# Kernel tuning notes

Measured on AMD Instinct MI355X. Metric: run time of the kernel, lower is better.

## Reference

```python
import jax, jax.numpy as jnp
import numpy as np

EPS = 1e-7  # K.epsilon()

_LC = np.zeros((3, 3, 3), np.float32)  # Levi-Civita for 1x1->1
_LC[0, 1, 2] = _LC[1, 2, 0] = _LC[2, 0, 1] = 1.0
_LC[0, 2, 1] = _LC[2, 1, 0] = _LC[1, 0, 2] = -1.0


def _ssp(x):
    # shifted softplus: log(0.5*exp(x)+0.5)
    return jnp.log(0.5 * jnp.exp(x) + 0.5)


def _radial(image, w1, b1, w2, b2):
    # Sequential([Dense(32), Dense(feat)]) -- linear Dense layers (no activation)
    return (image @ w1 + b1) @ w2 + b2  # (m, a, b, feat)


def setup_inputs() -> dict:
    key = jax.random.key(0)
    ks = jax.random.split(key, 16)
    M, A, RBF, F, SI, H = 4, 256, 64, 32, 32, 32
    inp = {}
    inp["image"] = jax.random.uniform(ks[0], (M, A, A, RBF), dtype=jnp.float32)
    inp["vectors"] = jax.random.normal(ks[1], (M, A, A, 3), dtype=jnp.float32)
    inp["feat0"] = jax.random.normal(ks[2], (M, A, F, 1), dtype=jnp.float32)
    inp["feat1"] = jax.random.normal(ks[3], (M, A, F, 3), dtype=jnp.float32)
    i = 4
    for rin in (0, 1):
        for fro in (0, 1):
            tag = f"{rin}{fro}"
            inp[f"w1_{tag}"] = jax.random.normal(ks[i], (RBF, H)) / np.sqrt(RBF).astype(np.float32)
            inp[f"b1_{tag}"] = jnp.zeros((H,), jnp.float32)
            i += 1
            inp[f"w2_{tag}"] = jax.random.normal(ks[i], (H, F)) / np.sqrt(np.float32(H))
            inp[f"b2_{tag}"] = jnp.zeros((F,), jnp.float32)
            i += 1
    inp["w_si0"] = jax.random.normal(ks[i], (SI, 2 * F)) / np.sqrt(np.float32(2 * F)); i += 1
    inp["w_si1"] = jax.random.normal(ks[i], (SI, 3 * F)) / np.sqrt(np.float32(3 * F)); i += 1
    inp["b_act0"] = jnp.zeros((SI,), jnp.float32)
    inp["b_act1"] = jnp.zeros((SI,), jnp.float32)
    return inp


def reference(image, vectors, feat0, feat1,
              w1_00, b1_00, w2_00, b2_00,
              w1_01, b1_01, w2_01, b2_01,
              w1_10, b1_10, w2_10, b2_10,
              w1_11, b1_11, w2_11, b2_11,
              w_si0, w_si1, b_act0, b_act1):
    # mask where |r_ab| < eps (self-pairs / padding)
    mask = (jnp.sqrt(jnp.sum(vectors * vectors, axis=-1)) < EPS)[..., None]  # (m,a,b,1)

    def filt0(w1, b1, w2, b2):
        return _radial(image, w1, b1, w2, b2)  # (m,a,b,F), implicit rep index of size 1

    def filt1(w1, b1, w2, b2):
        r = jnp.where(mask, 0.0, _radial(image, w1, b1, w2, b2))  # masked radial
        return vectors[:, :, :, None, :] * r[..., None]  # (m,a,b,F,3)

    f0_in0 = filt0(w1_00, b1_00, w2_00, b2_00)
    f1_in0 = filt1(w1_01, b1_01, w2_01, b2_01)
    f0_in1 = filt0(w1_10, b1_10, w2_10, b2_10)
    f1_in1 = filt1(w1_11, b1_11, w2_11, b2_11)

    # point convolution (sum over neighbor atoms b)
    out_0x0_0 = jnp.einsum('mabf,mbfj->mafj', f0_in0, feat0)   # (m,a,F,1)
    out_0x1_1 = jnp.einsum('mabfi,mbfj->mafi', f1_in0, feat0)  # (m,a,F,3)
    out_1x0_1 = jnp.einsum('mabf,mbfj->mafj', f0_in1, feat1)   # (m,a,F,3)
    cg0 = jnp.eye(3, dtype=image.dtype)[None]                  # (1,3,3): 1x1->0
    out_1x1_0 = jnp.einsum('ijk,mabfj,mbfk->mafi', cg0, f1_in1, feat1)  # (m,a,F,1)
    lc = jnp.asarray(_LC, image.dtype)                         # 1x1->1
    out_1x1_1 = jnp.einsum('ijk,mabfj,mbfk->mafi', lc, f1_in1, feat1)   # (m,a,F,3)

    # concat along channel dim per output RO
    cat0 = jnp.concatenate([out_0x0_0, out_1x1_0], axis=2)  # (m,a,2F,1)
    cat1 = jnp.concatenate([out_0x1_1, out_1x0_1, out_1x1_1], axis=2)  # (m,a,3F,3)

    # self-interaction: einsum('mafi,gf->maig') then transpose -> (m,a,g,i)
    si0 = jnp.einsum('mafi,gf->magi', cat0, w_si0)  # (m,a,SI,1)
    si1 = jnp.einsum('mafi,gf->magi', cat1, w_si1)  # (m,a,SI,3)

    # equivariant activation
    o0 = _ssp(si0 + b_act0[None, None, :, None])
    n1 = jnp.sqrt(jnp.maximum(jnp.sum(si1 * si1, axis=-1), EPS))  # norm_with_epsilon
    a1 = _ssp(n1 + b_act1)
    o1 = si1 * (a1 / n1)[..., None]
    return (o0, o1)
```

## Files before the change

kernel.cpp:

```cpp
#include <hip/hip_runtime.h>
#include <math.h>

#define M_ 4
#define A_ 256
#define RBF_ 64
#define F_ 32
#define H_ 32
#define SI_ 32
#define TF_ 128

typedef __attribute__((ext_vector_type(8))) short bf16x8;
typedef __attribute__((ext_vector_type(4))) float f32x4;
typedef __attribute__((ext_vector_type(3))) float f32x3;

__device__ __forceinline__ unsigned short f2bf(float f) {
  union { float f; unsigned u; } v; v.f = f;
  unsigned r = v.u + 0x7FFFu + ((v.u >> 16) & 1u);
  return (unsigned short)(r >> 16);
}

__device__ __forceinline__ unsigned pack2bf(float lo, float hi) {
  union { float f; unsigned u; } a, b; a.f = lo; b.f = hi;
  return __builtin_amdgcn_perm(b.u + 0x8000u, a.u + 0x8000u, 0x07060302u);
}

__device__ __forceinline__ float sspf(float x) {
  return fmaxf(x, 0.f) + log1pf(expf(-fabsf(x))) - 0.6931471805599453f;
}

__global__ __launch_bounds__(256) void combine_weights(
    const float* __restrict__ w1_00, const float* __restrict__ b1_00,
    const float* __restrict__ w2_00, const float* __restrict__ b2_00,
    const float* __restrict__ w1_01, const float* __restrict__ b1_01,
    const float* __restrict__ w2_01, const float* __restrict__ b2_01,
    const float* __restrict__ w1_10, const float* __restrict__ b1_10,
    const float* __restrict__ w2_10, const float* __restrict__ b2_10,
    const float* __restrict__ w1_11, const float* __restrict__ b1_11,
    const float* __restrict__ w2_11, const float* __restrict__ b2_11,
    unsigned short* __restrict__ wsT, float* __restrict__ bcw)
{
  const float* w1s[4] = {w1_00, w1_01, w1_10, w1_11};
  const float* b1s[4] = {b1_00, b1_01, b1_10, b1_11};
  const float* w2s[4] = {w2_00, w2_01, w2_10, w2_11};
  const float* b2s[4] = {b2_00, b2_01, b2_10, b2_11};
  int tid = blockIdx.x * 256 + threadIdx.x;
  int k   = tid >> 7;
  int tf  = tid & 127;
  int tag = tf >> 5, f = tf & 31;
  const float* w1 = w1s[tag];
  const float* w2 = w2s[tag];
  float s = 0.f;
  for (int h = 0; h < H_; ++h) s += w1[k * H_ + h] * w2[h * F_ + f];
  wsT[tf * 64 + k] = f2bf(s);
  if (tid < TF_) {
    const float* b1 = b1s[tag];
    const float* b2 = b2s[tag];
    float sb = b2[f];
    for (int h = 0; h < H_; ++h) sb += b1[h] * w2[h * F_ + f];
    bcw[tf] = sb;
  }
}

__global__ __launch_bounds__(512, 4) void conv_partial(
    const float* __restrict__ image, const float* __restrict__ vectors,
    const float* __restrict__ feat0, const float* __restrict__ feat1,
    const unsigned short* __restrict__ wsT, const float* __restrict__ bcw,
    float* __restrict__ part)
{
  __shared__ __align__(16) unsigned short sA[128 * 72];
  __shared__ float sV[128 * 3];

  const int t    = threadIdx.x;
  const int bid  = blockIdx.x;
  const int ma   = bid >> 1;
  const int half = bid & 1;
  const int m    = ma >> 8;
  const int l    = t & 63;
  const int n    = l & 15;
  const int quad = l >> 4;
  const int wu    = __builtin_amdgcn_readfirstlane(t >> 6);
  const int role  = (wu + ((bid & 3) << 1)) & 7;
  const int which = role & 1;
  const int tag   = role >> 1;
  const int ct    = tag * 2 + which;
  const int f     = which * 16 + n;

  const unsigned short* wr = wsT + (ct * 16 + n) * 64 + quad * 8;
  const bf16x8 w0 = *(const bf16x8*)(wr);
  const bf16x8 w1 = *(const bf16x8*)(wr + 32);
  const float  bc = bcw[ct * 16 + n];

  const float* imgH = image + ((size_t)ma * A_ + half * 128) * RBF_;
  #pragma unroll
  for (int i = 0; i < 2; ++i) {
    int g = t + 512 * i;
    int r = g >> 3, c8 = g & 7;
    const float* src = imgH + r * RBF_ + c8 * 8;
    float4 v0 = *(const float4*)(src);
    float4 v1 = *(const float4*)(src + 4);
    uint4 pk;
    pk.x = pack2bf(v0.x, v0.y);
    pk.y = pack2bf(v0.z, v0.w);
    pk.z = pack2bf(v1.x, v1.y);
    pk.w = pack2bf(v1.z, v1.w);
    *(uint4*)&sA[r * 72 + c8 * 8] = pk;
  }
  if (t < 384) sV[t] = vectors[((size_t)ma * A_ + half * 128) * 3 + t];

  const int b0q = half * 128 + quad * 4;
  const float* p0c = feat0 + (size_t)(m * A_ + b0q) * F_ + f;
  const float* p1c = feat1 + ((size_t)(m * A_ + b0q) * F_ + f) * 3;
  const float* svc = &sV[quad * 4 * 3];
  const unsigned short* aBc = &sA[n * 72 + quad * 8];

  float gx[2][4], gy[2][4], gz[2][4];
  float pA = 0.f, pB0 = 0.f, pB1 = 0.f, pB2 = 0.f;

#define PF(BUF) { \
    if (tag <= 1) { \
      _Pragma("unroll") \
      for (int r = 0; r < 4; ++r) gx[BUF][r] = p0c[r * F_]; \
    } else { \
      _Pragma("unroll") \
      for (int r = 0; r < 4; ++r) { \
        f32x3 v = *(const f32x3*)(p1c + r * (F_ * 3)); \
        gx[BUF][r] = v[0]; gy[BUF][r] = v[1]; gz[BUF][r] = v[2]; \
      } \
    } \
    p0c += 16 * F_; p1c += 16 * F_ * 3; }

#define BODY(AOFF, SOFF, GX, GY, GZ) { \
    const bf16x8 a0 = *(const bf16x8*)(aBc + (AOFF)); \
    const bf16x8 a1 = *(const bf16x8*)(aBc + (AOFF) + 32); \
    f32x4 acc = {bc, bc, bc, bc}; \
    acc = __builtin_amdgcn_mfma_f32_16x16x32_bf16(a0, w0, acc, 0, 0, 0); \
    acc = __builtin_amdgcn_mfma_f32_16x16x32_bf16(a1, w1, acc, 0, 0, 0); \
    if (tag == 0) {             \
      _Pragma("unroll") \
      for (int r = 0; r < 4; ++r) pA += acc[r] * GX[r]; \
    } else if (tag == 1) {      \
      _Pragma("unroll") \
      for (int r = 0; r < 4; ++r) { \
        const float s = acc[r] * GX[r]; \
        pB0 += svc[(SOFF) + r * 3 + 0] * s; \
        pB1 += svc[(SOFF) + r * 3 + 1] * s; \
        pB2 += svc[(SOFF) + r * 3 + 2] * s; \
      } \
    } else if (tag == 2) {      \
      _Pragma("unroll") \
      for (int r = 0; r < 4; ++r) { \
        const float Rr = acc[r]; \
        pB0 += Rr * GX[r]; pB1 += Rr * GY[r]; pB2 += Rr * GZ[r]; \
      } \
    } else {                    \
      _Pragma("unroll") \
      for (int r = 0; r < 4; ++r) { \
        const float Rr = acc[r]; \
        const float ax = GX[r], ay = GY[r], az = GZ[r]; \
        const float vx = svc[(SOFF) + r * 3 + 0]; \
        const float vy = svc[(SOFF) + r * 3 + 1]; \
        const float vz = svc[(SOFF) + r * 3 + 2]; \
        float d = vx * ax; d = fmaf(vy, ay, d); d = fmaf(vz, az, d); \
        pA = fmaf(Rr, d, pA); \
        float c0 = vy * az; c0 = fmaf(-vz, ay, c0); pB0 = fmaf(Rr, c0, pB0); \
        float c1 = vz * ax; c1 = fmaf(-vx, az, c1); pB1 = fmaf(Rr, c1, pB1); \
        float c2 = vx * ay; c2 = fmaf(-vy, ax, c2); pB2 = fmaf(Rr, c2, pB2); \
      } \
    } }

  PF(0)
  __syncthreads();

  #pragma unroll 1
  for (int it = 0; it < 4; ++it) {
    PF(1)
    BODY(0, 0, gx[0], gy[0], gz[0])
    if (it < 3) PF(0)
    BODY(1152, 48, gx[1], gy[1], gz[1])
    aBc += 2 * 1152;
    svc += 2 * 48;
  }

#define QRED(x) { x += __shfl_xor(x, 16); x += __shfl_xor(x, 32); }
  QRED(pA) QRED(pB0) QRED(pB1) QRED(pB2)
  if (quad == 0) {
    float* dst = part + ((size_t)ma * 2 + half) * 352;
    if (tag == 0) {
      dst[f] = pA;
    } else if (tag == 1) {
      f32x3 v = {pB0, pB1, pB2};
      *(f32x3*)&dst[64 + f * 3] = v;
    } else if (tag == 2) {
      f32x3 v = {pB0, pB1, pB2};
      *(f32x3*)&dst[160 + f * 3] = v;
    } else {
      dst[32 + f] = pA;
      f32x3 v = {pB0, pB1, pB2};
      *(f32x3*)&dst[256 + f * 3] = v;
    }
  }
}

__global__ __launch_bounds__(64) void si_epilogue(
    const float* __restrict__ part,
    const float* __restrict__ w_si0, const float* __restrict__ w_si1,
    const float* __restrict__ b_act0, const float* __restrict__ b_act1,
    float* __restrict__ out)
{
  __shared__ float cat[352];
  const int ma = blockIdx.x;
  const int t  = threadIdx.x;
  const float* pA = part + (size_t)ma * 704;
  const float* pB = pA + 352;
  for (int s = t; s < 352; s += 64) cat[s] = pA[s] + pB[s];
  __syncthreads();

  const int outBase = ma * SI_;
  if (t < 32) {
    const float* wr = w_si0 + t * 64;
    float s = 0.f;
    #pragma unroll 8
    for (int ff = 0; ff < 64; ++ff) s += cat[ff] * wr[ff];
    s += b_act0[t];
    out[outBase + t] = sspf(s);
  } else {
    int g = t - 32;
    const float* wr = w_si1 + g * 96;
    float s0 = 0.f, s1 = 0.f, s2 = 0.f;
    #pragma unroll 8
    for (int ff = 0; ff < 96; ++ff) {
      float wv = wr[ff];
      s0 += cat[64 + ff * 3 + 0] * wv;
      s1 += cat[64 + ff * 3 + 1] * wv;
      s2 += cat[64 + ff * 3 + 2] * wv;
    }
    float n2 = s0 * s0 + s1 * s1 + s2 * s2;
    float n1 = sqrtf(fmaxf(n2, 1e-7f));
    float a1 = sspf(n1 + b_act1[g]);
    float sc = a1 / n1;
    int ob = M_ * A_ * SI_ + (outBase + g) * 3;
    out[ob + 0] = s0 * sc;
    out[ob + 1] = s1 * sc;
    out[ob + 2] = s2 * sc;
  }
}

extern "C" void kernel_launch(void* const* d_in, const int* in_sizes, int n_in,
                              void* d_out, int out_size, void* d_ws, size_t ws_size,
                              hipStream_t stream) {
  const float* image   = (const float*)d_in[0];
  const float* vectors = (const float*)d_in[1];
  const float* feat0   = (const float*)d_in[2];
  const float* feat1   = (const float*)d_in[3];
  const float* w_si0   = (const float*)d_in[20];
  const float* w_si1   = (const float*)d_in[21];
  const float* b_act0  = (const float*)d_in[22];
  const float* b_act1  = (const float*)d_in[23];
  unsigned short* wsT = (unsigned short*)d_ws;
  float* bcw  = (float*)((char*)d_ws + 16384);
  float* part = (float*)((char*)d_ws + 32768);
  float* out  = (float*)d_out;

  combine_weights<<<32, 256, 0, stream>>>(
      (const float*)d_in[4],  (const float*)d_in[5],
      (const float*)d_in[6],  (const float*)d_in[7],
      (const float*)d_in[8],  (const float*)d_in[9],
      (const float*)d_in[10], (const float*)d_in[11],
      (const float*)d_in[12], (const float*)d_in[13],
      (const float*)d_in[14], (const float*)d_in[15],
      (const float*)d_in[16], (const float*)d_in[17],
      (const float*)d_in[18], (const float*)d_in[19],
      wsT, bcw);

  conv_partial<<<2 * M_ * A_, 512, 0, stream>>>(
      image, vectors, feat0, feat1, wsT, bcw, part);

  si_epilogue<<<M_ * A_, 64, 0, stream>>>(
      part, w_si0, w_si1, b_act0, b_act1, out);
}
```

Baseline: 161.3 us.

## Deepen feature prefetch to three buffers and stagger tile order per wave

The feature prefetch grows from two buffers to three, and the 8-step loop over b-tiles is fully unrolled. Each wave now starts at a different tile, offset by its wave index, which spreads LDS and global access across waves. Vector reads from shared memory become aligned float4 loads, and accumulations are written as explicit FMAs. The launch bound drops the minimum blocks per SM from 4 to 3, allowing more registers for the deeper buffering at the cost of possible lower occupancy.

```diff
diff --git a/kernel.cpp b/kernel.cpp
--- a/kernel.cpp
+++ b/kernel.cpp
@@ -61,14 +61,14 @@
   }
 }
 
-__global__ __launch_bounds__(512, 4) void conv_partial(
+__global__ __launch_bounds__(512, 3) void conv_partial(
     const float* __restrict__ image, const float* __restrict__ vectors,
     const float* __restrict__ feat0, const float* __restrict__ feat1,
     const unsigned short* __restrict__ wsT, const float* __restrict__ bcw,
     float* __restrict__ part)
 {
   __shared__ __align__(16) unsigned short sA[128 * 72];
-  __shared__ float sV[128 * 3];
+  __shared__ __align__(16) float sV[128 * 3];
 
   const int t    = threadIdx.x;
   const int bid  = blockIdx.x;
@@ -107,59 +107,73 @@
   }
   if (t < 384) sV[t] = vectors[((size_t)ma * A_ + half * 128) * 3 + t];
 
-  const int b0q = half * 128 + quad * 4;
-  const float* p0c = feat0 + (size_t)(m * A_ + b0q) * F_ + f;
-  const float* p1c = feat1 + ((size_t)(m * A_ + b0q) * F_ + f) * 3;
-  const float* svc = &sV[quad * 4 * 3];
-  const unsigned short* aBc = &sA[n * 72 + quad * 8];
-
-  float gx[2][4], gy[2][4], gz[2][4];
+  const int bq = half * 128 + quad * 4;
+  const float* p0b = feat0 + (size_t)(m * A_ + bq) * F_ + f;
+  const float* p1b = feat1 + ((size_t)(m * A_ + bq) * F_ + f) * 3;
+
+  float gx[3][4], gy[3][4], gz[3][4];
   float pA = 0.f, pB0 = 0.f, pB1 = 0.f, pB2 = 0.f;
 
-#define PF(BUF) { \
+#define PF(BUF, TJ) { \
+    const int _tj = (TJ); \
     if (tag <= 1) { \
-      _Pragma("unroll") \
-      for (int r = 0; r < 4; ++r) gx[BUF][r] = p0c[r * F_]; \
+      const float* pp = p0b + _tj * (16 * F_); \
+      _Pragma("unroll") \
+      for (int r = 0; r < 4; ++r) gx[BUF][r] = pp[r * F_]; \
     } else { \
-      _Pragma("unroll") \
-      for (int r = 0; r < 4; ++r) { \
-        f32x3 v = *(const f32x3*)(p1c + r * (F_ * 3)); \
+      const float* pp = p1b + _tj * (16 * F_ * 3); \
+      _Pragma("unroll") \
+      for (int r = 0; r < 4; ++r) { \
+        f32x3 v = *(const f32x3*)(pp + r * (F_ * 3)); \
         gx[BUF][r] = v[0]; gy[BUF][r] = v[1]; gz[BUF][r] = v[2]; \
       } \
-    } \
-    p0c += 16 * F_; p1c += 16 * F_ * 3; }
-
-#define BODY(AOFF, SOFF, GX, GY, GZ) { \
-    const bf16x8 a0 = *(const bf16x8*)(aBc + (AOFF)); \
-    const bf16x8 a1 = *(const bf16x8*)(aBc + (AOFF) + 32); \
+    } }
+
+#define BODY(BUF, TJ) { \
+    const int _tj = (TJ); \
+    const unsigned short* ap = &sA[(_tj * 16 + n) * 72 + quad * 8]; \
+    const bf16x8 a0 = *(const bf16x8*)(ap); \
+    const bf16x8 a1 = *(const bf16x8*)(ap + 32); \
     f32x4 acc = {bc, bc, bc, bc}; \
     acc = __builtin_amdgcn_mfma_f32_16x16x32_bf16(a0, w0, acc, 0, 0, 0); \
     acc = __builtin_amdgcn_mfma_f32_16x16x32_bf16(a1, w1, acc, 0, 0, 0); \
     if (tag == 0) {             \
       _Pragma("unroll") \
-      for (int r = 0; r < 4; ++r) pA += acc[r] * GX[r]; \
+      for (int r = 0; r < 4; ++r) pA += acc[r] * gx[BUF][r]; \
     } else if (tag == 1) {      \
-      _Pragma("unroll") \
-      for (int r = 0; r < 4; ++r) { \
-        const float s = acc[r] * GX[r]; \
-        pB0 += svc[(SOFF) + r * 3 + 0] * s; \
-        pB1 += svc[(SOFF) + r * 3 + 1] * s; \
-        pB2 += svc[(SOFF) + r * 3 + 2] * s; \
+      const float* vp = &sV[_tj * 48 + quad * 12]; \
+      float4 q0 = *(const float4*)(vp); \
+      float4 q1 = *(const float4*)(vp + 4); \
+      float4 q2 = *(const float4*)(vp + 8); \
+      const float vvv[12] = {q0.x,q0.y,q0.z,q0.w,q1.x,q1.y,q1.z,q1.w, \
+                             q2.x,q2.y,q2.z,q2.w}; \
+      _Pragma("unroll") \
+      for (int r = 0; r < 4; ++r) { \
+        const float s = acc[r] * gx[BUF][r]; \
+        pB0 = fmaf(vvv[r*3+0], s, pB0); \
+        pB1 = fmaf(vvv[r*3+1], s, pB1); \
+        pB2 = fmaf(vvv[r*3+2], s, pB2); \
       } \
     } else if (tag == 2) {      \
       _Pragma("unroll") \
       for (int r = 0; r < 4; ++r) { \
         const float Rr = acc[r]; \
-        pB0 += Rr * GX[r]; pB1 += Rr * GY[r]; pB2 += Rr * GZ[r]; \
+        pB0 = fmaf(Rr, gx[BUF][r], pB0); \
+        pB1 = fmaf(Rr, gy[BUF][r], pB1); \
+        pB2 = fmaf(Rr, gz[BUF][r], pB2); \
       } \
     } else {                    \
+      const float* vp = &sV[_tj * 48 + quad * 12]; \
+      float4 q0 = *(const float4*)(vp); \
+      float4 q1 = *(const float4*)(vp + 4); \
+      float4 q2 = *(const float4*)(vp + 8); \
+      const float vvv[12] = {q0.x,q0.y,q0.z,q0.w,q1.x,q1.y,q1.z,q1.w, \
+                             q2.x,q2.y,q2.z,q2.w}; \
       _Pragma("unroll") \
       for (int r = 0; r < 4; ++r) { \
         const float Rr = acc[r]; \
-        const float ax = GX[r], ay = GY[r], az = GZ[r]; \
-        const float vx = svc[(SOFF) + r * 3 + 0]; \
-        const float vy = svc[(SOFF) + r * 3 + 1]; \
-        const float vz = svc[(SOFF) + r * 3 + 2]; \
+        const float ax = gx[BUF][r], ay = gy[BUF][r], az = gz[BUF][r]; \
+        const float vx = vvv[r*3+0], vy = vvv[r*3+1], vz = vvv[r*3+2]; \
         float d = vx * ax; d = fmaf(vy, ay, d); d = fmaf(vz, az, d); \
         pA = fmaf(Rr, d, pA); \
         float c0 = vy * az; c0 = fmaf(-vz, ay, c0); pB0 = fmaf(Rr, c0, pB0); \
@@ -168,17 +182,15 @@
       } \
     } }
 
-  PF(0)
+  PF(0, (wu + 0) & 7)
+  PF(1, (wu + 1) & 7)
+  PF(2, (wu + 2) & 7)
   __syncthreads();
 
-  #pragma unroll 1
-  for (int it = 0; it < 4; ++it) {
-    PF(1)
-    BODY(0, 0, gx[0], gy[0], gz[0])
-    if (it < 3) PF(0)
-    BODY(1152, 48, gx[1], gy[1], gz[1])
-    aBc += 2 * 1152;
-    svc += 2 * 48;
+  #pragma unroll
+  for (int j = 0; j < 8; ++j) {
+    BODY(j % 3, (wu + j) & 7)
+    if (j < 5) PF(j % 3, (wu + j + 3) & 7)
   }
 
 #define QRED(x) { x += __shfl_xor(x, 16); x += __shfl_xor(x, 32); }
```

New measurement: 166.3 us. 1.03x slower.
